# Optimization experiments

Measured on AMD Instinct MI355X. Metric: run time of the kernel, lower is better.

The kernel has to match this reference:

```python
import jax, jax.numpy as jnp
import numpy as np

B, S, D = 1, 2048, 4096
H, KV, HD = 32, 8, 128
REP = H // KV            # 4, GQA repeat factor
THETA = 500000.0
NEG = -1e9               # stand-in for -inf in additive causal mask


def _rope(x, cos, sin):
    # x: [B,S,h,HD]; complex rotation on interleaved (even,odd) pairs,
    # matching torch.view_as_complex on [..., HD/2, 2]
    xr, xi = x[..., 0::2], x[..., 1::2]
    c = cos[None, :, None, :]
    s = sin[None, :, None, :]
    out_r = xr * c - xi * s
    out_i = xr * s + xi * c
    return jnp.stack([out_r, out_i], axis=-1).reshape(x.shape)


def setup_inputs() -> dict:
    key = jax.random.key(0)
    ks = jax.random.split(key, 6)
    x = jax.random.normal(ks[0], (B, S, D), dtype=jnp.float32)
    # torch nn.Linear weights are [out, in]
    sc = 1.0 / np.sqrt(D)
    wq = jax.random.normal(ks[1], (H * HD, D), dtype=jnp.float32) * sc
    wk = jax.random.normal(ks[2], (KV * HD, D), dtype=jnp.float32) * sc
    wv = jax.random.normal(ks[3], (KV * HD, D), dtype=jnp.float32) * sc
    wo = jax.random.normal(ks[4], (D, H * HD), dtype=jnp.float32) * sc
    # RoPE freqs_cis = exp(i * t * theta_f), stored as cos/sin [S, HD/2]
    freqs = 1.0 / (THETA ** (jnp.arange(0, HD, 2, dtype=jnp.float32) / HD))
    ang = jnp.outer(jnp.arange(S, dtype=jnp.float32), freqs)
    cos, sin = jnp.cos(ang), jnp.sin(ang)
    cache = jnp.zeros((2, B, S, KV, HD), dtype=jnp.float32)
    mask = jnp.where(jnp.tril(jnp.ones((S, S), dtype=bool)), 0.0, NEG).astype(jnp.float32)
    return {"x": x, "wq": wq, "wk": wk, "wv": wv, "wo": wo,
            "cos": cos, "sin": sin, "cache": cache, "mask": mask,
            "start_pos": 0}


def reference(x, wq, wk, wv, wo, cos, sin, cache, mask, start_pos):
    b, s, _ = x.shape
    xq = (x @ wq.T).reshape(b, s, H, HD)
    xk = (x @ wk.T).reshape(b, s, KV, HD)
    xv = (x @ wv.T).reshape(b, s, KV, HD)
    xq = _rope(xq, cos, sin)
    xk = _rope(xk, cos, sin)
    # functional KV-cache write
    cache = cache.at[0, :b, start_pos:start_pos + s].set(xk)
    cache = cache.at[1, :b, start_pos:start_pos + s].set(xv)
    keys = cache[0, :b, :start_pos + s]    # [b,T,KV,HD]
    values = cache[1, :b, :start_pos + s]  # [b,T,KV,HD]
    # GQA: head h = kv*REP + r (repeat_interleave ordering)
    q = xq.reshape(b, s, KV, REP, HD)
    scores = jnp.einsum('bskrd,btkd->bkrst', q, keys) / jnp.sqrt(jnp.float32(HD))
    scores = scores + mask[None, None, None]           # [b,KV,REP,s,T]
    p = jax.nn.softmax(scores.astype(jnp.float32), axis=-1).astype(x.dtype)
    out = jnp.einsum('bkrst,btkd->bskrd', p, values).reshape(b, s, H * HD)
    return out @ wo.T
```

## Files before the change

kernel.cpp:

```cpp
#include <hip/hip_runtime.h>
#include <stdint.h>

typedef __bf16 bf16_8 __attribute__((ext_vector_type(8)));
typedef __bf16 bf16_4 __attribute__((ext_vector_type(4)));
typedef float  f32x4  __attribute__((ext_vector_type(4)));

#define B_  1
#define S_  2048
#define D_  4096
#define H_  32
#define KV_ 8
#define HD_ 128

__device__ inline void gload_lds16(const void* g, void* l) {
  __builtin_amdgcn_global_load_lds((const __attribute__((address_space(1))) void*)g,
                                   (__attribute__((address_space(3))) void*)l, 16, 0, 0);
}

__global__ __launch_bounds__(256) void cvt_all(const float* __restrict__ x,
                                               const float* __restrict__ wq,
                                               const float* __restrict__ wk,
                                               const float* __restrict__ wv,
                                               __bf16* __restrict__ dst) {
  int i = blockIdx.x * 256 + threadIdx.x;
  const float* s;
  int j = i;
  if (j < 2097152) s = x;
  else if ((j -= 2097152) < 4194304) s = wq;
  else if ((j -= 4194304) < 1048576) s = wk;
  else { j -= 1048576; s = wv; }
  float4 v = ((const float4*)s)[j];
  bf16_4 o = { (__bf16)v.x, (__bf16)v.y, (__bf16)v.z, (__bf16)v.w };
  ((bf16_4*)dst)[i] = o;
}

__global__ __launch_bounds__(256) void gemm_qkv(const __bf16* __restrict__ xb,
                                                const __bf16* __restrict__ wqb,
                                                const __bf16* __restrict__ wkb,
                                                const __bf16* __restrict__ wvb,
                                                const float* __restrict__ cosT,
                                                const float* __restrict__ sinT,
                                                __bf16* __restrict__ Qb,
                                                __bf16* __restrict__ Kb,
                                                __bf16* __restrict__ Vt) {
  __shared__ __bf16 As[128 * 32];
  __shared__ __bf16 Bs[128 * 32];
  const int nb = blockIdx.x, mb = blockIdx.y;
  const __bf16* W; int wrow0;
  if (nb < 32)      { W = wqb; wrow0 = nb * 128; }
  else if (nb < 40) { W = wkb; wrow0 = (nb - 32) * 128; }
  else              { W = wvb; wrow0 = (nb - 40) * 128; }
  const int tid = threadIdx.x, lane = tid & 63, wv = tid >> 6;
  const int wm = wv >> 1, wn = wv & 1;
  const int srow = lane >> 2, scol = (lane & 3) * 8;

  const __bf16* Ag0 = xb + (size_t)(mb * 128 + 2 * wv * 16 + srow) * D_ + scol;
  const __bf16* Bg0 = W  + (size_t)(wrow0 + 2 * wv * 16 + srow) * D_ + scol;
  __bf16* Al = As + 2 * wv * 512;
  __bf16* Bl = Bs + 2 * wv * 512;

  const f32x4 zv = {0.f, 0.f, 0.f, 0.f};
  f32x4 acc[4][4];
#pragma unroll
  for (int i = 0; i < 4; ++i)
#pragma unroll
    for (int j = 0; j < 4; ++j) acc[i][j] = zv;

  for (int k0 = 0; k0 < D_; k0 += 32) {
    gload_lds16(Ag0 + k0, Al);
    gload_lds16(Ag0 + (size_t)16 * D_ + k0, Al + 512);
    gload_lds16(Bg0 + k0, Bl);
    gload_lds16(Bg0 + (size_t)16 * D_ + k0, Bl + 512);
    __syncthreads();
    bf16_8 af[4], bfr[4];
#pragma unroll
    for (int i = 0; i < 4; ++i)
      af[i] = *(const bf16_8*)&As[(wm * 64 + i * 16 + (lane & 15)) * 32 + (lane >> 4) * 8];
#pragma unroll
    for (int j = 0; j < 4; ++j)
      bfr[j] = *(const bf16_8*)&Bs[(wn * 64 + j * 16 + (lane & 15)) * 32 + (lane >> 4) * 8];
#pragma unroll
    for (int i = 0; i < 4; ++i)
#pragma unroll
      for (int j = 0; j < 4; ++j)
        acc[i][j] = __builtin_amdgcn_mfma_f32_16x16x32_bf16(af[i], bfr[j], acc[i][j], 0, 0, 0);
    __syncthreads();
  }

#pragma unroll
  for (int i = 0; i < 4; ++i) {
    int row0 = mb * 128 + wm * 64 + i * 16 + (lane >> 4) * 4;
#pragma unroll
    for (int j = 0; j < 4; ++j) {
      int cl = wn * 64 + j * 16 + (lane & 15);
      if (nb < 40) {
        int f = cl >> 1;
        float sgn = (cl & 1) ? 1.f : -1.f;
        f32x4 v = acc[i][j];
        float o[4];
#pragma unroll
        for (int r = 0; r < 4; ++r) {
          float p = __shfl_xor(v[r], 1);
          float c = cosT[(size_t)(row0 + r) * 64 + f];
          float s = sinT[(size_t)(row0 + r) * 64 + f];
          o[r] = v[r] * c + sgn * p * s;
        }
        if (nb < 32) {
          int colg = nb * 128 + cl;
#pragma unroll
          for (int r = 0; r < 4; ++r)
            Qb[(size_t)(row0 + r) * D_ + colg] = (__bf16)o[r];
        } else {
          int colg = (nb - 32) * 128 + cl;
#pragma unroll
          for (int r = 0; r < 4; ++r)
            Kb[(size_t)(row0 + r) * 1024 + colg] = (__bf16)o[r];
        }
      } else {
        int colg = (nb - 40) * 128 + cl;
        bf16_4 pv = { (__bf16)acc[i][j][0], (__bf16)acc[i][j][1],
                      (__bf16)acc[i][j][2], (__bf16)acc[i][j][3] };
        *(bf16_4*)&Vt[(size_t)colg * S_ + row0] = pv;
      }
    }
  }
}

__global__ __launch_bounds__(256) void gemm_out(const __bf16* __restrict__ Ob,
                                                const __bf16* __restrict__ wob,
                                                float* __restrict__ Of) {
  __shared__ __bf16 As[128 * 32];
  __shared__ __bf16 Bs[128 * 32];
  const int nb = blockIdx.x, mb = blockIdx.y;
  const int tid = threadIdx.x, lane = tid & 63, wv = tid >> 6;
  const int wm = wv >> 1, wn = wv & 1;
  const int srow = lane >> 2, scol = (lane & 3) * 8;

  const __bf16* Ag0 = Ob  + (size_t)(mb * 128 + 2 * wv * 16 + srow) * D_ + scol;
  const __bf16* Bg0 = wob + (size_t)(nb * 128 + 2 * wv * 16 + srow) * D_ + scol;
  __bf16* Al = As + 2 * wv * 512;
  __bf16* Bl = Bs + 2 * wv * 512;

  const f32x4 zv = {0.f, 0.f, 0.f, 0.f};
  f32x4 acc[4][4];
#pragma unroll
  for (int i = 0; i < 4; ++i)
#pragma unroll
    for (int j = 0; j < 4; ++j) acc[i][j] = zv;

  for (int k0 = 0; k0 < D_; k0 += 32) {
    gload_lds16(Ag0 + k0, Al);
    gload_lds16(Ag0 + (size_t)16 * D_ + k0, Al + 512);
    gload_lds16(Bg0 + k0, Bl);
    gload_lds16(Bg0 + (size_t)16 * D_ + k0, Bl + 512);
    __syncthreads();
    bf16_8 af[4], bfr[4];
#pragma unroll
    for (int i = 0; i < 4; ++i)
      af[i] = *(const bf16_8*)&As[(wm * 64 + i * 16 + (lane & 15)) * 32 + (lane >> 4) * 8];
#pragma unroll
    for (int j = 0; j < 4; ++j)
      bfr[j] = *(const bf16_8*)&Bs[(wn * 64 + j * 16 + (lane & 15)) * 32 + (lane >> 4) * 8];
#pragma unroll
    for (int i = 0; i < 4; ++i)
#pragma unroll
      for (int j = 0; j < 4; ++j)
        acc[i][j] = __builtin_amdgcn_mfma_f32_16x16x32_bf16(af[i], bfr[j], acc[i][j], 0, 0, 0);
    __syncthreads();
  }

#pragma unroll
  for (int i = 0; i < 4; ++i) {
    int row0 = mb * 128 + wm * 64 + i * 16 + (lane >> 4) * 4;
#pragma unroll
    for (int j = 0; j < 4; ++j) {
      int colg = nb * 128 + wn * 64 + j * 16 + (lane & 15);
#pragma unroll
      for (int r = 0; r < 4; ++r)
        Of[(size_t)(row0 + r) * D_ + colg] = acc[i][j][r];
    }
  }
}

#define COMPUTE_TILE(ACC, MR, LR, AQ, QB0, DOMASK, KSB, VSB)                       \
  {                                                                                \
    f32x4 sfr_[4];                                                                 \
    __builtin_amdgcn_s_setprio(1);                                                 \
    _Pragma("unroll")                                                              \
    for (int nf = 0; nf < 4; ++nf) {                                               \
      f32x4 c_ = zv;                                                               \
      _Pragma("unroll")                                                            \
      for (int ks = 0; ks < 4; ++ks) {                                             \
        int n_ = nf * 16 + (lane & 15);                                            \
        int bo_ = (n_ * 256 + (ks * 32 + (lane >> 4) * 8) * 2) ^ ((n_ & 7) << 4);  \
        bf16_8 bk_ = *(const bf16_8*)((char*)(KSB) + bo_);                         \
        c_ = __builtin_amdgcn_mfma_f32_16x16x32_bf16(bk_, AQ[ks], c_, 0, 0, 0);    \
      }                                                                            \
      sfr_[nf] = c_;                                                               \
    }                                                                              \
    __builtin_amdgcn_s_setprio(0);                                                 \
    const int myq_ = (QB0) + w4 * 16 + (lane & 15);                                \
    float pmn_[4];                                                                 \
    _Pragma("unroll")                                                              \
    for (int nf = 0; nf < 4; ++nf) {                                               \
      float t_ = -3e38f;                                                           \
      _Pragma("unroll")                                                            \
      for (int r = 0; r < 4; ++r) {                                                \
        int kcol_ = kb * 64 + nf * 16 + (lane >> 4) * 4 + r;                       \
        float v_ = sfr_[nf][r];                                                    \
        if ((DOMASK) && kcol_ > myq_) v_ = -1e9f;                                  \
        sfr_[nf][r] = v_;                                                          \
        t_ = fmaxf(t_, v_);                                                        \
      }                                                                            \
      pmn_[nf] = t_;                                                               \
    }                                                                              \
    float pm_ = fmaxf(fmaxf(pmn_[0], pmn_[1]), fmaxf(pmn_[2], pmn_[3]));           \
    pm_ = fmaxf(pm_, __shfl_xor(pm_, 16));                                         \
    pm_ = fmaxf(pm_, __shfl_xor(pm_, 32));                                         \
    if (!__all(pm_ <= MR + 8.f)) {                                                 \
      float mn_ = fmaxf(MR, pm_);                                                  \
      float rs_ = __expf(MR - mn_);                                                \
      MR = mn_;                                                                    \
      LR *= rs_;                                                                   \
      float rsb_[4];                                                               \
      _Pragma("unroll")                                                            \
      for (int r = 0; r < 4; ++r)                                                  \
        rsb_[r] = __shfl(rs_, (lane & 48) | ((lane >> 4) * 4 + r));                \
      _Pragma("unroll")                                                            \
      for (int d = 0; d < 8; ++d)                                                  \
        _Pragma("unroll")                                                          \
        for (int r = 0; r < 4; ++r) ACC[d][r] *= rsb_[r];                          \
    }                                                                              \
    float psn_[4];                                                                 \
    _Pragma("unroll")                                                              \
    for (int nf = 0; nf < 4; ++nf) {                                               \
      bf16_4 pk_;                                                                  \
      float t_ = 0.f;                                                              \
      _Pragma("unroll")                                                            \
      for (int r = 0; r < 4; ++r) {                                                \
        float p_ = __expf(sfr_[nf][r] - MR);                                       \
        t_ += p_;                                                                  \
        pk_[r] = (__bf16)p_;                                                       \
      }                                                                            \
      psn_[nf] = t_;                                                               \
      int bo_ = ((lane & 15) * 128 + nf * 32 + (lane >> 4) * 8) ^                  \
                (((lane & 15) & 7) << 4);                                          \
      *(bf16_4*)((char*)(&Ps[wid][0]) + bo_) = pk_;                                \
    }                                                                              \
    float ps_ = (psn_[0] + psn_[1]) + (psn_[2] + psn_[3]);                         \
    ps_ += __shfl_xor(ps_, 16);                                                    \
    ps_ += __shfl_xor(ps_, 32);                                                    \
    LR += ps_;                                                                     \
    bf16_8 ap_[2];                                                                 \
    _Pragma("unroll")                                                              \
    for (int ks = 0; ks < 2; ++ks) {                                               \
      int bo_ = ((lane & 15) * 128 + (ks * 32 + (lane >> 4) * 8) * 2) ^            \
                (((lane & 15) & 7) << 4);                                          \
      ap_[ks] = *(const bf16_8*)((char*)(&Ps[wid][0]) + bo_);                      \
    }                                                                              \
    __builtin_amdgcn_s_setprio(1);                                                 \
    _Pragma("unroll")                                                              \
    for (int d = 0; d < 8; ++d) {                                                  \
      _Pragma("unroll")                                                            \
      for (int ks = 0; ks < 2; ++ks) {                                             \
        int dr_ = d * 16 + (lane & 15);                                            \
        int bo_ = (dr_ * 128 + (ks * 32 + (lane >> 4) * 8) * 2) ^ ((dr_ & 7) << 4);\
        bf16_8 bv_ = *(const bf16_8*)((char*)(VSB) + bo_);                         \
        ACC[d] = __builtin_amdgcn_mfma_f32_16x16x32_bf16(ap_[ks], bv_, ACC[d], 0, 0, 0); \
      }                                                                            \
    }                                                                              \
    __builtin_amdgcn_s_setprio(0);                                                 \
  }

__global__ __launch_bounds__(512, 4) void attn_k(const __bf16* __restrict__ Qb,
                                                 const __bf16* __restrict__ Kb,
                                                 const __bf16* __restrict__ Vt,
                                                 const float* __restrict__ wo,
                                                 __bf16* __restrict__ wob,
                                                 __bf16* __restrict__ Ob) {
  __shared__ __bf16 Ks[2][64 * 128];
  __shared__ __bf16 Vs[2][128 * 64];
  __shared__ __bf16 Ps[8][16 * 64];

  {
    const float4* src = (const float4*)wo;
    bf16_4* dst = (bf16_4*)wob;
    int t0 = blockIdx.x * 512 + threadIdx.x;
#pragma unroll
    for (int u = 0; u < 16; ++u) {
      int idx = t0 + u * 262144;
      float4 v = src[idx];
      bf16_4 o = { (__bf16)v.x, (__bf16)v.y, (__bf16)v.z, (__bf16)v.w };
      dst[idx] = o;
    }
  }

  const int bid = blockIdx.x;
  const int kvh = bid & 7;
  const int hsel = (bid >> 3) & 3;
  const int h = kvh * 4 + hsel;
  const int xraw = (bid >> 5) & 7;
  const int x = (bid >> 8) ? (15 - xraw) : xraw;
  const int qlo = x, qhi = 31 - x;
  const int tid = threadIdx.x, lane = tid & 63, wid = tid >> 6;
  const int w4 = wid & 3;
  const int qt = (wid < 4) ? qhi : qlo;

  const float sc = 0.08838834764831845f;

  bf16_8 aq[4];
#pragma unroll
  for (int ks = 0; ks < 4; ++ks) {
    int rr = qt * 64 + w4 * 16 + (lane & 15);
    int cc = h * 128 + ks * 32 + (lane >> 4) * 8;
    bf16_8 t = *(const bf16_8*)&Qb[(size_t)rr * D_ + cc];
#pragma unroll
    for (int e = 0; e < 8; ++e) aq[ks][e] = (__bf16)((float)t[e] * sc);
  }

  const f32x4 zv = {0.f, 0.f, 0.f, 0.f};
  f32x4 acc[8];
#pragma unroll
  for (int d = 0; d < 8; ++d) acc[d] = zv;
  float mr = -3e38f, lr = 0.f;

#define KSTAGE(BUF, KB)                                                            \
  {                                                                                \
    _Pragma("unroll")                                                              \
    for (int u = 0; u < 2; ++u) {                                                  \
      int chunk = (u * 8 + wid) * 64 + lane;                                       \
      int row = chunk >> 4, p8 = chunk & 15;                                       \
      gload_lds16(&Kb[(size_t)((KB) * 64 + row) * 1024 + kvh * 128 + (p8 ^ (row & 7)) * 8], \
                  &Ks[BUF][(u * 8 + wid) * 512]);                                  \
    }                                                                              \
    _Pragma("unroll")                                                              \
    for (int u = 0; u < 2; ++u) {                                                  \
      int chunk = (u * 8 + wid) * 64 + lane;                                       \
      int vr = chunk >> 3, p8 = chunk & 7;                                         \
      gload_lds16(&Vt[(size_t)(kvh * 128 + vr) * S_ + (KB) * 64 + (p8 ^ (vr & 7)) * 8], \
                  &Vs[BUF][(u * 8 + wid) * 512]);                                  \
    }                                                                              \
  }

  KSTAGE(0, 0);
  asm volatile("s_waitcnt vmcnt(0)" ::: "memory");
  __syncthreads();

  for (int kb = 0; kb <= qhi; ++kb) {
    const int cur = kb & 1;
    if (kb < qhi) KSTAGE(cur ^ 1, kb + 1);
    const __bf16* ksb = &Ks[cur][0];
    const __bf16* vsb = &Vs[cur][0];
    if (kb <= qt) COMPUTE_TILE(acc, mr, lr, aq, qt * 64, (kb == qt), ksb, vsb);
    if (kb < qhi) {
      asm volatile("s_waitcnt vmcnt(0)" ::: "memory");
      __syncthreads();
    }
  }

  float inv[4];
#pragma unroll
  for (int r = 0; r < 4; ++r)
    inv[r] = 1.0f / __shfl(lr, (lane & 48) | ((lane >> 4) * 4 + r));
#pragma unroll
  for (int d = 0; d < 8; ++d) {
#pragma unroll
    for (int r = 0; r < 4; ++r) {
      size_t row = (size_t)(qt * 64 + w4 * 16 + (lane >> 4) * 4 + r);
      Ob[row * D_ + h * 128 + d * 16 + (lane & 15)] = (__bf16)(acc[d][r] * inv[r]);
    }
  }
}

extern "C" void kernel_launch(void* const* d_in, const int* in_sizes, int n_in,
                              void* d_out, int out_size, void* d_ws, size_t ws_size,
                              hipStream_t stream) {
  const float* x    = (const float*)d_in[0];
  const float* wq   = (const float*)d_in[1];
  const float* wk   = (const float*)d_in[2];
  const float* wv   = (const float*)d_in[3];
  const float* wo   = (const float*)d_in[4];
  const float* cosT = (const float*)d_in[5];
  const float* sinT = (const float*)d_in[6];
  float* out = (float*)d_out;
  char* ws = (char*)d_ws;

  __bf16* xb  = (__bf16*)(ws + 0);
  __bf16* wqb = (__bf16*)(ws + 16777216);
  __bf16* wkb = (__bf16*)(ws + 50331648);
  __bf16* wvb = (__bf16*)(ws + 58720256);
  __bf16* wob = (__bf16*)(ws + 67108864);
  __bf16* Qb  = (__bf16*)(ws + 100663296);
  __bf16* Kb  = (__bf16*)(ws + 117440512);
  __bf16* Vt  = (__bf16*)(ws + 121634816);
  __bf16* Ob  = xb;

  cvt_all<<<32768, 256, 0, stream>>>(x, wq, wk, wv, xb);

  gemm_qkv<<<dim3(48, 16), 256, 0, stream>>>(xb, wqb, wkb, wvb, cosT, sinT, Qb, Kb, Vt);

  attn_k<<<512, 512, 0, stream>>>(Qb, Kb, Vt, wo, wob, Ob);

  gemm_out<<<dim3(32, 16), 256, 0, stream>>>(Ob, wob, out);
}
```

Baseline: 353.5 us.

## Split attention into one query tile per block and widen bf16 conversion

The attention kernel no longer pairs a high and a low query tile in one 512-thread block that shares K/V loads. It now launches 1024 blocks of 256 threads, each handling one query tile, with heavy tiles scheduled first. Double buffering of the K/V LDS stages is dropped for a single buffer with explicit syncs before and after each load, which cuts LDS use and may raise occupancy. The cost is lost load/compute overlap and twice the K/V traffic per query tile. Separately, the fp32-to-bf16 conversion kernel becomes a grid-stride loop that converts 8 elements per thread over 2048 blocks.

```diff
diff --git a/kernel.cpp b/kernel.cpp
--- a/kernel.cpp
+++ b/kernel.cpp
@@ -22,16 +22,20 @@
                                                const float* __restrict__ wk,
                                                const float* __restrict__ wv,
                                                __bf16* __restrict__ dst) {
-  int i = blockIdx.x * 256 + threadIdx.x;
-  const float* s;
-  int j = i;
-  if (j < 2097152) s = x;
-  else if ((j -= 2097152) < 4194304) s = wq;
-  else if ((j -= 4194304) < 1048576) s = wk;
-  else { j -= 1048576; s = wv; }
-  float4 v = ((const float4*)s)[j];
-  bf16_4 o = { (__bf16)v.x, (__bf16)v.y, (__bf16)v.z, (__bf16)v.w };
-  ((bf16_4*)dst)[i] = o;
+  const int total = 4194304;
+  for (int i = blockIdx.x * 256 + threadIdx.x; i < total; i += 524288) {
+    const float* s;
+    int j = i;
+    if (j < 1048576) s = x;
+    else if ((j -= 1048576) < 2097152) s = wq;
+    else if ((j -= 2097152) < 524288) s = wk;
+    else { j -= 524288; s = wv; }
+    float4 a = ((const float4*)s)[j * 2];
+    float4 b = ((const float4*)s)[j * 2 + 1];
+    bf16_8 o = { (__bf16)a.x, (__bf16)a.y, (__bf16)a.z, (__bf16)a.w,
+                 (__bf16)b.x, (__bf16)b.y, (__bf16)b.z, (__bf16)b.w };
+    ((bf16_8*)dst)[i] = o;
+  }
 }
 
 __global__ __launch_bounds__(256) void gemm_qkv(const __bf16* __restrict__ xb,
@@ -199,7 +203,7 @@
       sfr_[nf] = c_;                                                               \
     }                                                                              \
     __builtin_amdgcn_s_setprio(0);                                                 \
-    const int myq_ = (QB0) + w4 * 16 + (lane & 15);                                \
+    const int myq_ = (QB0) + w * 16 + (lane & 15);                                 \
     float pmn_[4];                                                                 \
     _Pragma("unroll")                                                              \
     for (int nf = 0; nf < 4; ++nf) {                                               \
@@ -245,7 +249,7 @@
       psn_[nf] = t_;                                                               \
       int bo_ = ((lane & 15) * 128 + nf * 32 + (lane >> 4) * 8) ^                  \
                 (((lane & 15) & 7) << 4);                                          \
-      *(bf16_4*)((char*)(&Ps[wid][0]) + bo_) = pk_;                                \
+      *(bf16_4*)((char*)(&Ps[w][0]) + bo_) = pk_;                                  \
     }                                                                              \
     float ps_ = (psn_[0] + psn_[1]) + (psn_[2] + psn_[3]);                         \
     ps_ += __shfl_xor(ps_, 16);                                                    \
@@ -256,7 +260,7 @@
     for (int ks = 0; ks < 2; ++ks) {                                               \
       int bo_ = ((lane & 15) * 128 + (ks * 32 + (lane >> 4) * 8) * 2) ^            \
                 (((lane & 15) & 7) << 4);                                          \
-      ap_[ks] = *(const bf16_8*)((char*)(&Ps[wid][0]) + bo_);                      \
+      ap_[ks] = *(const bf16_8*)((char*)(&Ps[w][0]) + bo_);                        \
     }                                                                              \
     __builtin_amdgcn_s_setprio(1);                                                 \
     _Pragma("unroll")                                                              \
@@ -272,20 +276,20 @@
     __builtin_amdgcn_s_setprio(0);                                                 \
   }
 
-__global__ __launch_bounds__(512, 4) void attn_k(const __bf16* __restrict__ Qb,
+__global__ __launch_bounds__(256, 4) void attn_k(const __bf16* __restrict__ Qb,
                                                  const __bf16* __restrict__ Kb,
                                                  const __bf16* __restrict__ Vt,
                                                  const float* __restrict__ wo,
                                                  __bf16* __restrict__ wob,
                                                  __bf16* __restrict__ Ob) {
-  __shared__ __bf16 Ks[2][64 * 128];
-  __shared__ __bf16 Vs[2][128 * 64];
-  __shared__ __bf16 Ps[8][16 * 64];
+  __shared__ __bf16 Ks[64 * 128];
+  __shared__ __bf16 Vs[128 * 64];
+  __shared__ __bf16 Ps[4][16 * 64];
 
   {
     const float4* src = (const float4*)wo;
     bf16_4* dst = (bf16_4*)wob;
-    int t0 = blockIdx.x * 512 + threadIdx.x;
+    int t0 = blockIdx.x * 256 + threadIdx.x;
 #pragma unroll
     for (int u = 0; u < 16; ++u) {
       int idx = t0 + u * 262144;
@@ -299,19 +303,15 @@
   const int kvh = bid & 7;
   const int hsel = (bid >> 3) & 3;
   const int h = kvh * 4 + hsel;
-  const int xraw = (bid >> 5) & 7;
-  const int x = (bid >> 8) ? (15 - xraw) : xraw;
-  const int qlo = x, qhi = 31 - x;
-  const int tid = threadIdx.x, lane = tid & 63, wid = tid >> 6;
-  const int w4 = wid & 3;
-  const int qt = (wid < 4) ? qhi : qlo;
+  const int qt = 31 - (bid >> 5);
+  const int tid = threadIdx.x, lane = tid & 63, w = tid >> 6;
 
   const float sc = 0.08838834764831845f;
 
   bf16_8 aq[4];
 #pragma unroll
   for (int ks = 0; ks < 4; ++ks) {
-    int rr = qt * 64 + w4 * 16 + (lane & 15);
+    int rr = qt * 64 + w * 16 + (lane & 15);
     int cc = h * 128 + ks * 32 + (lane >> 4) * 8;
     bf16_8 t = *(const bf16_8*)&Qb[(size_t)rr * D_ + cc];
 #pragma unroll
@@ -324,37 +324,33 @@
   for (int d = 0; d < 8; ++d) acc[d] = zv;
   float mr = -3e38f, lr = 0.f;
 
-#define KSTAGE(BUF, KB)                                                            \
+#define KSTAGE(KB)                                                                 \
   {                                                                                \
     _Pragma("unroll")                                                              \
-    for (int u = 0; u < 2; ++u) {                                                  \
-      int chunk = (u * 8 + wid) * 64 + lane;                                       \
+    for (int u = 0; u < 4; ++u) {                                                  \
+      int chunk = (u * 4 + w) * 64 + lane;                                         \
       int row = chunk >> 4, p8 = chunk & 15;                                       \
       gload_lds16(&Kb[(size_t)((KB) * 64 + row) * 1024 + kvh * 128 + (p8 ^ (row & 7)) * 8], \
-                  &Ks[BUF][(u * 8 + wid) * 512]);                                  \
-    }                                                                              \
-    _Pragma("unroll")                                                              \
-    for (int u = 0; u < 2; ++u) {                                                  \
-      int chunk = (u * 8 + wid) * 64 + lane;                                       \
+                  &Ks[(u * 4 + w) * 512]);                                         \
+    }                                                                              \
+    _Pragma("unroll")                                                              \
+    for (int u = 0; u < 4; ++u) {                                                  \
+      int chunk = (u * 4 + w) * 64 + lane;                                         \
       int vr = chunk >> 3, p8 = chunk & 7;                                         \
       gload_lds16(&Vt[(size_t)(kvh * 128 + vr) * S_ + (KB) * 64 + (p8 ^ (vr & 7)) * 8], \
-                  &Vs[BUF][(u * 8 + wid) * 512]);                                  \
-    }                                                                              \
-  }
-
-  KSTAGE(0, 0);
-  asm volatile("s_waitcnt vmcnt(0)" ::: "memory");
-  __syncthreads();
-
-  for (int kb = 0; kb <= qhi; ++kb) {
-    const int cur = kb & 1;
-    if (kb < qhi) KSTAGE(cur ^ 1, kb + 1);
-    const __bf16* ksb = &Ks[cur][0];
-    const __bf16* vsb = &Vs[cur][0];
-    if (kb <= qt) COMPUTE_TILE(acc, mr, lr, aq, qt * 64, (kb == qt), ksb, vsb);
-    if (kb < qhi) {
-      asm volatile("s_waitcnt vmcnt(0)" ::: "memory");
+                  &Vs[(u * 4 + w) * 512]);                                         \
+    }                                                                              \
+  }
+
+  KSTAGE(0);
+
+  for (int kb = 0; kb <= qt; ++kb) {
+    asm volatile("s_waitcnt vmcnt(0)" ::: "memory");
+    __syncthreads();
+    COMPUTE_TILE(acc, mr, lr, aq, qt * 64, (kb == qt), Ks, Vs);
+    if (kb < qt) {
       __syncthreads();
+      KSTAGE(kb + 1);
     }
   }
 
@@ -366,7 +362,7 @@
   for (int d = 0; d < 8; ++d) {
 #pragma unroll
     for (int r = 0; r < 4; ++r) {
-      size_t row = (size_t)(qt * 64 + w4 * 16 + (lane >> 4) * 4 + r);
+      size_t row = (size_t)(qt * 64 + w * 16 + (lane >> 4) * 4 + r);
       Ob[row * D_ + h * 128 + d * 16 + (lane & 15)] = (__bf16)(acc[d][r] * inv[r]);
     }
   }
@@ -395,11 +391,11 @@
   __bf16* Vt  = (__bf16*)(ws + 121634816);
   __bf16* Ob  = xb;
 
-  cvt_all<<<32768, 256, 0, stream>>>(x, wq, wk, wv, xb);
+  cvt_all<<<2048, 256, 0, stream>>>(x, wq, wk, wv, xb);
 
   gemm_qkv<<<dim3(48, 16), 256, 0, stream>>>(xb, wqb, wkb, wvb, cosT, sinT, Qb, Kb, Vt);
 
-  attn_k<<<512, 512, 0, stream>>>(Qb, Kb, Vt, wo, wob, Ob);
+  attn_k<<<1024, 256, 0, stream>>>(Qb, Kb, Vt, wo, wob, Ob);
 
   gemm_out<<<dim3(32, 16), 256, 0, stream>>>(Ob, wob, out);
 }
```

Measured after the change: 418.4 us. 18.4% more time.
